# Optimization experiments

Hardware: AMD Instinct MI355X
Metric: run time of the kernel (lower is better)

Reference implementation:

```python
import jax, jax.numpy as jnp
import numpy as np

N_SOURCE = 200_000
N_TARGET = 20_000
SOURCE_DIM = 1024
EMBED_DIM = 32
TARGET_DIM = 16
N_EDGES = 4_000_000


def setup_inputs() -> dict:
    key = jax.random.key(0)
    k0, k1, k2, k3, k4, k5 = jax.random.split(key, 6)
    source_feat = jax.random.normal(k0, (N_SOURCE, SOURCE_DIM), dtype=jnp.float32)
    # positive per-node normalizers (as in the original x_norm), kept away from 0
    x_norm = jax.random.uniform(k1, (N_SOURCE,), dtype=jnp.float32) + 0.5
    # edges: row 0 = source node id, row 1 = target id, sorted by target so that
    # range_list gives contiguous per-target slices
    src = jax.random.randint(k2, (N_EDGES,), 0, N_SOURCE, dtype=jnp.int64)
    tgt = jnp.sort(jax.random.randint(k3, (N_EDGES,), 0, N_TARGET, dtype=jnp.int64))
    edge_index = jnp.stack([src, tgt], axis=0)
    # range_list[i] = (start, end) of target i's edge slice
    counts = jnp.bincount(tgt, length=N_TARGET)
    ends = jnp.cumsum(counts)
    starts = ends - counts
    range_list = jnp.stack([starts, ends], axis=1).astype(jnp.int64)
    # learned params
    embed = jax.random.normal(k4, (SOURCE_DIM, EMBED_DIM), dtype=jnp.float32)
    weight = jax.random.normal(k5, (EMBED_DIM, TARGET_DIM), dtype=jnp.float32) / EMBED_DIM
    return {
        "source_feat": source_feat,
        "x_norm": x_norm,
        "edge_index": edge_index,
        "range_list": range_list,
        "embed": embed,
        "weight": weight,
    }


def reference(source_feat, x_norm, edge_index, range_list, embed, weight):
    # 1) dense embedding projection + per-node normalization
    x = jnp.matmul(source_feat, embed)          # [Ns, embed_dim]
    x = x / x_norm[:, None]
    # 2) hierarchical conv: gather source features along edges, mean-aggregate
    #    per target (edges are target-sorted, so segment_sum over edge_index[1]
    #    equals the original range_list slice-sum), then project.
    n_target = range_list.shape[0]
    tmp = x[edge_index[0]]                      # [E, embed_dim] irregular gather
    out = jax.ops.segment_sum(tmp, edge_index[1], num_segments=n_target)
    deg = (range_list[:, 1] - range_list[:, 0]).astype(x.dtype)
    out = out / jnp.maximum(deg, 1.0)[:, None]  # mean over each target's edges
    return jnp.matmul(out, weight)              # [Nt, target_dim]
```

## Files before the change

### kernel.cpp

```cpp
#include <hip/hip_runtime.h>
#include <stdint.h>

#define NS 200000
#define NT 20000
#define SD 1024
#define ED 32
#define TD 16
#define NE 4000000

typedef __bf16 bf16x8 __attribute__((ext_vector_type(8)));
typedef float  f32x4  __attribute__((ext_vector_type(4)));
typedef int    i32x4  __attribute__((ext_vector_type(4)));
typedef unsigned int u32;
typedef unsigned short u16;

__device__ inline u16 f2bf_u(float f) {
    u32 u = __builtin_bit_cast(u32, f);
    u += 0x7fffu + ((u >> 16) & 1u);
    return (u16)(u >> 16);
}

__global__ void bfrag_kernel(const float* __restrict__ embed,
                             u16* __restrict__ bfrag) {
    int tid = blockIdx.x * 64 + threadIdx.x;
    int kc = tid >> 7;
    int nt = (tid >> 6) & 1;
    int l  = tid & 63;
    int g = l >> 4, c = l & 15;
    int k0 = kc * 32 + g * 8;
    u16* dst = bfrag + ((size_t)(kc * 2 + nt) * 64 + l) * 8;
#pragma unroll
    for (int j = 0; j < 8; ++j) {
        dst[j] = f2bf_u(embed[(size_t)(k0 + j) * ED + nt * 16 + c]);
    }
}

__global__ __launch_bounds__(256) void proj_kernel(
    const float* __restrict__ A, const float* __restrict__ xnorm,
    const u16* __restrict__ bfrag, u16* __restrict__ xout) {
    int w = threadIdx.x >> 6;
    int l = threadIdx.x & 63;
    int m = blockIdx.x * 4 + w;
    int g = l >> 4, c = l & 15;

    const float* arow = A + (size_t)(m * 16 + c) * SD + g * 8;
    const i32x4* bf = (const i32x4*)bfrag;

    f32x4 acc0 = {0.f, 0.f, 0.f, 0.f};
    f32x4 acc1 = {0.f, 0.f, 0.f, 0.f};

#pragma unroll 4
    for (int kc = 0; kc < 32; ++kc) {
        const float* ap = arow + kc * 32;
        f32x4 a0 = *(const f32x4*)(ap);
        f32x4 a1 = *(const f32x4*)(ap + 4);
        bf16x8 a;
        a[0] = (__bf16)a0[0]; a[1] = (__bf16)a0[1];
        a[2] = (__bf16)a0[2]; a[3] = (__bf16)a0[3];
        a[4] = (__bf16)a1[0]; a[5] = (__bf16)a1[1];
        a[6] = (__bf16)a1[2]; a[7] = (__bf16)a1[3];
        bf16x8 b0 = __builtin_bit_cast(bf16x8, bf[(kc * 2 + 0) * 64 + l]);
        bf16x8 b1 = __builtin_bit_cast(bf16x8, bf[(kc * 2 + 1) * 64 + l]);
        acc0 = __builtin_amdgcn_mfma_f32_16x16x32_bf16(a, b0, acc0, 0, 0, 0);
        acc1 = __builtin_amdgcn_mfma_f32_16x16x32_bf16(a, b1, acc1, 0, 0, 0);
    }

#pragma unroll
    for (int r = 0; r < 4; ++r) {
        int grow = m * 16 + g * 4 + r;
        float inv = 1.0f / xnorm[grow];
        __bf16 v0 = (__bf16)(acc0[r] * inv);
        __bf16 v1 = (__bf16)(acc1[r] * inv);
        xout[(size_t)grow * ED + c]      = __builtin_bit_cast(u16, v0);
        xout[(size_t)grow * ED + 16 + c] = __builtin_bit_cast(u16, v1);
    }
}

__global__ __launch_bounds__(256) void agg_kernel(
    const u16* __restrict__ xbf, const int* __restrict__ edge_src,
    const int* __restrict__ range_list, const float* __restrict__ weight,
    float* __restrict__ out) {
    __shared__ float meanS[4][ED];
    __shared__ float Wl[ED * TD];

    int tid = threadIdx.x;
    Wl[tid]       = weight[tid];
    Wl[tid + 256] = weight[tid + 256];

    int w = tid >> 6, l = tid & 63;
    int t = blockIdx.x * 4 + w;
    int start = range_list[2 * t];
    int end   = range_list[2 * t + 1];
    int grp = l >> 2;
    int qd  = l & 3;

    float acc[8];
#pragma unroll
    for (int j = 0; j < 8; ++j) acc[j] = 0.f;

    for (int e0 = start; e0 < end; e0 += 16) {
        int e = e0 + grp;
        if (e < end) {
            int sid = edge_src[e];
            i32x4 v = *(const i32x4*)(xbf + (size_t)sid * ED + qd * 8);
#pragma unroll
            for (int j = 0; j < 4; ++j) {
                u32 u = (u32)v[j];
                acc[2 * j]     += __builtin_bit_cast(float, u << 16);
                acc[2 * j + 1] += __builtin_bit_cast(float, u & 0xffff0000u);
            }
        }
    }

#pragma unroll
    for (int m = 4; m <= 32; m <<= 1) {
#pragma unroll
        for (int j = 0; j < 8; ++j) acc[j] += __shfl_xor(acc[j], m);
    }

    int deg = end - start;
    float inv = 1.0f / (float)(deg > 0 ? deg : 1);
    if (l < 4) {
#pragma unroll
        for (int j = 0; j < 8; ++j) meanS[w][qd * 8 + j] = acc[j] * inv;
    }
    __syncthreads();

    if (l < TD) {
        float o = 0.f;
#pragma unroll
        for (int dd = 0; dd < ED; ++dd) o += meanS[w][dd] * Wl[dd * TD + l];
        out[(size_t)t * TD + l] = o;
    }
}

extern "C" void kernel_launch(void* const* d_in, const int* in_sizes, int n_in,
                              void* d_out, int out_size, void* d_ws, size_t ws_size,
                              hipStream_t stream) {
    const float* source_feat = (const float*)d_in[0];
    const float* x_norm      = (const float*)d_in[1];
    const int*   edge_index  = (const int*)d_in[2];
    const int*   range_list  = (const int*)d_in[3];
    const float* embed       = (const float*)d_in[4];
    const float* weight      = (const float*)d_in[5];
    float* out = (float*)d_out;

    u16* bfrag = (u16*)d_ws;
    u16* xbf   = (u16*)((char*)d_ws + 65536);

    hipLaunchKernelGGL(bfrag_kernel, dim3(64),   dim3(64),  0, stream, embed, bfrag);
    hipLaunchKernelGGL(proj_kernel,  dim3(3125), dim3(256), 0, stream,
                       source_feat, x_norm, bfrag, xbf);
    hipLaunchKernelGGL(agg_kernel,   dim3(5000), dim3(256), 0, stream,
                       xbf, edge_index, range_list, weight, out);
}
```

Before: 238.1 us.

## Fold weight into embed so projection and aggregation run at 16 dims

Precomputes embed@weight (1024x16) and uses it as the MFMA B operand, so the projection writes 16-wide bf16 rows instead of 32-wide. This is valid because mean aggregation is linear and commutes with the final matmul. The change halves the size of the intermediate and the gathered bytes per edge, and removes the shared-memory epilogue matmul from the aggregation kernel. In exchange, the combined weights are rounded to bf16, which changes rounding slightly.

```diff
diff --git a/kernel.cpp b/kernel.cpp
--- a/kernel.cpp
+++ b/kernel.cpp
@@ -20,19 +20,17 @@
     return (u16)(u >> 16);
 }
 
-__global__ void bfrag_kernel(const float* __restrict__ embed,
+__global__ void pfrag_kernel(const float* __restrict__ embed,
+                             const float* __restrict__ weight,
                              u16* __restrict__ bfrag) {
-    int tid = blockIdx.x * 64 + threadIdx.x;
-    int kc = tid >> 7;
-    int nt = (tid >> 6) & 1;
-    int l  = tid & 63;
-    int g = l >> 4, c = l & 15;
-    int k0 = kc * 32 + g * 8;
-    u16* dst = bfrag + ((size_t)(kc * 2 + nt) * 64 + l) * 8;
+    int tid = blockIdx.x * 256 + threadIdx.x;
+    int k = tid >> 4;
+    int c = tid & 15;
+    float p = 0.f;
 #pragma unroll
-    for (int j = 0; j < 8; ++j) {
-        dst[j] = f2bf_u(embed[(size_t)(k0 + j) * ED + nt * 16 + c]);
-    }
+    for (int d = 0; d < ED; ++d) p += embed[(size_t)k * ED + d] * weight[d * TD + c];
+    int kc = k >> 5, r = k & 31, g = r >> 3, j = r & 7;
+    bfrag[((size_t)(kc * 64) + g * 16 + c) * 8 + j] = f2bf_u(p);
 }
 
 __global__ __launch_bounds__(256) void proj_kernel(
@@ -46,8 +44,7 @@
     const float* arow = A + (size_t)(m * 16 + c) * SD + g * 8;
     const i32x4* bf = (const i32x4*)bfrag;
 
-    f32x4 acc0 = {0.f, 0.f, 0.f, 0.f};
-    f32x4 acc1 = {0.f, 0.f, 0.f, 0.f};
+    f32x4 acc = {0.f, 0.f, 0.f, 0.f};
 
 #pragma unroll 4
     for (int kc = 0; kc < 32; ++kc) {
@@ -59,50 +56,38 @@
         a[2] = (__bf16)a0[2]; a[3] = (__bf16)a0[3];
         a[4] = (__bf16)a1[0]; a[5] = (__bf16)a1[1];
         a[6] = (__bf16)a1[2]; a[7] = (__bf16)a1[3];
-        bf16x8 b0 = __builtin_bit_cast(bf16x8, bf[(kc * 2 + 0) * 64 + l]);
-        bf16x8 b1 = __builtin_bit_cast(bf16x8, bf[(kc * 2 + 1) * 64 + l]);
-        acc0 = __builtin_amdgcn_mfma_f32_16x16x32_bf16(a, b0, acc0, 0, 0, 0);
-        acc1 = __builtin_amdgcn_mfma_f32_16x16x32_bf16(a, b1, acc1, 0, 0, 0);
+        bf16x8 b = __builtin_bit_cast(bf16x8, bf[kc * 64 + l]);
+        acc = __builtin_amdgcn_mfma_f32_16x16x32_bf16(a, b, acc, 0, 0, 0);
     }
 
 #pragma unroll
     for (int r = 0; r < 4; ++r) {
         int grow = m * 16 + g * 4 + r;
         float inv = 1.0f / xnorm[grow];
-        __bf16 v0 = (__bf16)(acc0[r] * inv);
-        __bf16 v1 = (__bf16)(acc1[r] * inv);
-        xout[(size_t)grow * ED + c]      = __builtin_bit_cast(u16, v0);
-        xout[(size_t)grow * ED + 16 + c] = __builtin_bit_cast(u16, v1);
+        __bf16 v = (__bf16)(acc[r] * inv);
+        xout[(size_t)grow * TD + c] = __builtin_bit_cast(u16, v);
     }
 }
 
 __global__ __launch_bounds__(256) void agg_kernel(
     const u16* __restrict__ xbf, const int* __restrict__ edge_src,
-    const int* __restrict__ range_list, const float* __restrict__ weight,
-    float* __restrict__ out) {
-    __shared__ float meanS[4][ED];
-    __shared__ float Wl[ED * TD];
-
-    int tid = threadIdx.x;
-    Wl[tid]       = weight[tid];
-    Wl[tid + 256] = weight[tid + 256];
-
-    int w = tid >> 6, l = tid & 63;
+    const int* __restrict__ range_list, float* __restrict__ out) {
+    int w = threadIdx.x >> 6, l = threadIdx.x & 63;
     int t = blockIdx.x * 4 + w;
     int start = range_list[2 * t];
     int end   = range_list[2 * t + 1];
-    int grp = l >> 2;
-    int qd  = l & 3;
+    int grp = l >> 1;
+    int hd  = l & 1;
 
     float acc[8];
 #pragma unroll
     for (int j = 0; j < 8; ++j) acc[j] = 0.f;
 
-    for (int e0 = start; e0 < end; e0 += 16) {
+    for (int e0 = start; e0 < end; e0 += 32) {
         int e = e0 + grp;
         if (e < end) {
             int sid = edge_src[e];
-            i32x4 v = *(const i32x4*)(xbf + (size_t)sid * ED + qd * 8);
+            i32x4 v = *(const i32x4*)(xbf + (size_t)sid * TD + hd * 8);
 #pragma unroll
             for (int j = 0; j < 4; ++j) {
                 u32 u = (u32)v[j];
@@ -113,24 +98,19 @@
     }
 
 #pragma unroll
-    for (int m = 4; m <= 32; m <<= 1) {
+    for (int m = 2; m <= 32; m <<= 1) {
 #pragma unroll
         for (int j = 0; j < 8; ++j) acc[j] += __shfl_xor(acc[j], m);
     }
 
-    int deg = end - start;
-    float inv = 1.0f / (float)(deg > 0 ? deg : 1);
-    if (l < 4) {
-#pragma unroll
-        for (int j = 0; j < 8; ++j) meanS[w][qd * 8 + j] = acc[j] * inv;
-    }
-    __syncthreads();
-
-    if (l < TD) {
-        float o = 0.f;
-#pragma unroll
-        for (int dd = 0; dd < ED; ++dd) o += meanS[w][dd] * Wl[dd * TD + l];
-        out[(size_t)t * TD + l] = o;
+    if (l < 2) {
+        int deg = end - start;
+        float inv = 1.0f / (float)(deg > 0 ? deg : 1);
+        f32x4 o0 = {acc[0] * inv, acc[1] * inv, acc[2] * inv, acc[3] * inv};
+        f32x4 o1 = {acc[4] * inv, acc[5] * inv, acc[6] * inv, acc[7] * inv};
+        float* dst = out + (size_t)t * TD + hd * 8;
+        *(f32x4*)(dst)     = o0;
+        *(f32x4*)(dst + 4) = o1;
     }
 }
 
@@ -146,11 +126,12 @@
     float* out = (float*)d_out;
 
     u16* bfrag = (u16*)d_ws;
-    u16* xbf   = (u16*)((char*)d_ws + 65536);
+    u16* xbf   = (u16*)((char*)d_ws + 32768);
 
-    hipLaunchKernelGGL(bfrag_kernel, dim3(64),   dim3(64),  0, stream, embed, bfrag);
+    hipLaunchKernelGGL(pfrag_kernel, dim3(64),   dim3(256), 0, stream,
+                       embed, weight, bfrag);
     hipLaunchKernelGGL(proj_kernel,  dim3(3125), dim3(256), 0, stream,
                        source_feat, x_norm, bfrag, xbf);
     hipLaunchKernelGGL(agg_kernel,   dim3(5000), dim3(256), 0, stream,
-                       xbf, edge_index, range_list, weight, out);
+                       xbf, edge_index, edge_index ? (const int*)d_in[3] : nullptr, out);
 }
```

After: 250.5 us. 1.05x slower.
